# Kernel optimization log

Measured on AMD Instinct MI355X. Metric: run time of the kernel, lower is better.

Reference implementation:

```python
import jax, jax.numpy as jnp
import numpy as np

B, N, F_IN, F_OUT = 8, 2048, 64, 64
ALPHA = 0.2  # LeakyReLU negative slope


def setup_inputs() -> dict:
    key = jax.random.key(0)
    k_in, k_adj, k_w, k_a1, k_a2 = jax.random.split(key, 5)
    inp = jax.random.normal(k_in, (B, N, F_IN), dtype=jnp.float32)
    adj = (jax.random.uniform(k_adj, (B, N, N)) < 0.05).astype(jnp.float32)
    # xavier_uniform with gain=sqrt(2)
    def xavier(k, shape):
        fan_in, fan_out = shape[0], shape[1]
        bound = np.sqrt(2.0) * np.sqrt(6.0 / (fan_in + fan_out))
        return jax.random.uniform(k, shape, jnp.float32, -bound, bound)
    W = xavier(k_w, (F_IN, F_OUT))
    a1 = xavier(k_a1, (F_OUT, 1))
    a2 = xavier(k_a2, (F_OUT, 1))
    bias = jnp.full((N, F_OUT), 0.1, dtype=jnp.float32)
    return {"input": inp, "adj": adj, "W": W, "a1": a1, "a2": a2, "bias": bias}


def reference(input, adj, W, a1, a2, bias):
    # h: [B, N, F_OUT]
    h = jnp.einsum("bnf,fo->bno", input, W)
    f1 = h @ a1          # [B, N, 1]
    f2 = h @ a2          # [B, N, 1]
    e = jax.nn.leaky_relu(f1 + jnp.swapaxes(f2, 1, 2), negative_slope=ALPHA)  # [B, N, N]
    # NOTE: original multiplies adj elementwise (not -inf mask) and softmaxes over dim=1
    attention = jax.nn.softmax(adj * e, axis=1)
    h_prime = jnp.einsum("bij,bjo->bio", attention, h) + bias  # bias broadcasts over batch
    h_prime = h_prime + input  # in_features == out_features, no downsample
    return jax.nn.elu(h_prime)
```

## Files before the change

### kernel.cpp

```cpp
#include <hip/hip_runtime.h>
#include <cstdint>
#include <cstddef>

#define Bn 8
#define Nn 2048
#define Fn 64
#define ALPHA 0.2f

typedef __attribute__((ext_vector_type(8))) short  s8frag;
typedef __attribute__((ext_vector_type(4))) float  f4frag;

__device__ __forceinline__ float lrelu(float x) { return fmaxf(x, ALPHA * x); }
__device__ __forceinline__ float elu(float x)   { return x > 0.f ? x : __expf(x) - 1.f; }
__device__ __forceinline__ unsigned short bfr(float f) {
    unsigned u = __float_as_uint(f);
    u += 0x7fffu + ((u >> 16) & 1u);
    return (unsigned short)(u >> 16);
}

__global__ __launch_bounds__(256) void k1_h_f(
        const float* __restrict__ inp, const float* __restrict__ W,
        const float* __restrict__ a1, const float* __restrict__ a2,
        float* __restrict__ h, float* __restrict__ f1, float* __restrict__ f2) {
    __shared__ float Wl[Fn * Fn];
    __shared__ float inr[4 * Fn];
    int t = threadIdx.x;
    for (int k = t; k < Fn * Fn; k += 256) Wl[k] = W[k];
    size_t row0 = (size_t)blockIdx.x * 4;
    inr[t] = inp[row0 * Fn + t];
    __syncthreads();
    int r = t >> 6, o = t & 63;
    const float* irow = &inr[r * Fn];
    float acc = 0.f;
#pragma unroll
    for (int f = 0; f < Fn; ++f) acc = fmaf(irow[f], Wl[f * Fn + o], acc);
    size_t row = row0 + r;
    h[row * Fn + o] = acc;
    float p = acc * a1[o];
    float q = acc * a2[o];
#pragma unroll
    for (int off = 32; off > 0; off >>= 1) {
        p += __shfl_down(p, off, 64);
        q += __shfl_down(q, off, 64);
    }
    if (o == 0) { f1[row] = p; f2[row] = q; }
}

__global__ __launch_bounds__(256) void k1b_max(
        const float* __restrict__ f1, float* __restrict__ f1max) {
    int b = blockIdx.x, t = threadIdx.x;
    float m = -3.4e38f;
    for (int i = t; i < Nn; i += 256) m = fmaxf(m, f1[b * Nn + i]);
#pragma unroll
    for (int off = 32; off > 0; off >>= 1) m = fmaxf(m, __shfl_down(m, off, 64));
    __shared__ float sm[4];
    if ((t & 63) == 0) sm[t >> 6] = m;
    __syncthreads();
    if (t == 0) f1max[b] = fmaxf(fmaxf(sm[0], sm[1]), fmaxf(sm[2], sm[3]));
}

__global__ __launch_bounds__(512) void k2a_dense(
        const float* __restrict__ adj, const float* __restrict__ f1,
        const float* __restrict__ f2, const float* __restrict__ f1max_p,
        float* __restrict__ Dsum, unsigned short* __restrict__ P) {
    int b = blockIdx.x;
    int j0 = blockIdx.y * 256;
    int i0 = blockIdx.z * 128;
    int w = threadIdx.x >> 6, lane = threadIdx.x & 63;
    float f1max = f1max_p[b];
    float4 f2v = *(const float4*)&f2[b * Nn + j0 + 4 * lane];
    float Mf0 = fmaxf(lrelu(f1max + f2v.x), 0.f);
    float Mf1 = fmaxf(lrelu(f1max + f2v.y), 0.f);
    float Mf2 = fmaxf(lrelu(f1max + f2v.z), 0.f);
    float Mf3 = fmaxf(lrelu(f1max + f2v.w), 0.f);
    float s0 = 0.f, s1 = 0.f, s2 = 0.f, s3 = 0.f;
    const float* abase = adj + ((size_t)b * Nn) * Nn + j0 + 4 * lane;
    unsigned short* pbase = P + ((size_t)b * Nn) * Nn + j0 + 4 * lane;
    const float* f1b = f1 + b * Nn;

    for (int g = 0; g < 4; ++g) {
        int r0 = i0 + w + 32 * g;
        float4 av0 = *(const float4*)(abase + (size_t)(r0 +  0) * Nn);
        float4 av1 = *(const float4*)(abase + (size_t)(r0 +  8) * Nn);
        float4 av2 = *(const float4*)(abase + (size_t)(r0 + 16) * Nn);
        float4 av3 = *(const float4*)(abase + (size_t)(r0 + 24) * Nn);
        float fi0 = f1b[r0], fi1 = f1b[r0 + 8], fi2 = f1b[r0 + 16], fi3 = f1b[r0 + 24];
#define PROC(AV, FI, IROW)                                                     \
        {                                                                      \
            float e0 = __expf((AV.x != 0.f ? lrelu((FI) + f2v.x) : 0.f) - Mf0);\
            float e1 = __expf((AV.y != 0.f ? lrelu((FI) + f2v.y) : 0.f) - Mf1);\
            float e2 = __expf((AV.z != 0.f ? lrelu((FI) + f2v.z) : 0.f) - Mf2);\
            float e3 = __expf((AV.w != 0.f ? lrelu((FI) + f2v.w) : 0.f) - Mf3);\
            s0 += e0; s1 += e1; s2 += e2; s3 += e3;                            \
            uint2 pk;                                                          \
            pk.x = (unsigned)bfr(e0) | ((unsigned)bfr(e1) << 16);              \
            pk.y = (unsigned)bfr(e2) | ((unsigned)bfr(e3) << 16);              \
            *(uint2*)(pbase + (size_t)(IROW) * Nn) = pk;                       \
        }
        PROC(av0, fi0, r0 +  0)
        PROC(av1, fi1, r0 +  8)
        PROC(av2, fi2, r0 + 16)
        PROC(av3, fi3, r0 + 24)
#undef PROC
    }
    __shared__ float sred[8][256];
    sred[w][4 * lane + 0] = s0;
    sred[w][4 * lane + 1] = s1;
    sred[w][4 * lane + 2] = s2;
    sred[w][4 * lane + 3] = s3;
    __syncthreads();
    if (threadIdx.x < 256) {
        int c = threadIdx.x;
        float v = 0.f;
#pragma unroll
        for (int k = 0; k < 8; ++k) v += sred[k][c];
        atomicAdd(&Dsum[b * Nn + j0 + c], v);
    }
}

__global__ __launch_bounds__(256) void k2b_scale_T(
        const float* __restrict__ h, const float* __restrict__ Dsum,
        unsigned short* __restrict__ hTs) {
    int b = blockIdx.x;
    int j0 = blockIdx.y * 64;
    int t = threadIdx.x;
    __shared__ float Lh[64][68];
    __shared__ float Rsh[64];
    if (t < 64) Rsh[t] = 1.f / Dsum[b * Nn + j0 + t];
#pragma unroll
    for (int q = 0; q < 4; ++q) {
        int fi = t + 256 * q;
        int jj = fi >> 4, oq = fi & 15;
        float4 v = *(const float4*)(h + ((size_t)(b * Nn + j0 + jj)) * Fn + oq * 4);
        *(float4*)&Lh[jj][oq * 4] = v;
    }
    __syncthreads();
    int o = t >> 2, jg = (t & 3) * 16;
    unsigned wbuf[8];
#pragma unroll
    for (int s2 = 0; s2 < 8; ++s2) {
        int j = jg + 2 * s2;
        unsigned lo16 = bfr(Lh[j][o] * Rsh[j]);
        unsigned hi16 = bfr(Lh[j + 1][o] * Rsh[j + 1]);
        wbuf[s2] = lo16 | (hi16 << 16);
    }
    unsigned short* dst = hTs + ((size_t)(b * Fn + o)) * Nn + j0 + jg;
    *(uint4*)dst       = make_uint4(wbuf[0], wbuf[1], wbuf[2], wbuf[3]);
    *(uint4*)(dst + 8) = make_uint4(wbuf[4], wbuf[5], wbuf[6], wbuf[7]);
}

__global__ __launch_bounds__(256) void k3_gemm(
        const unsigned short* __restrict__ P, const unsigned short* __restrict__ hTs,
        const float* __restrict__ inp, const float* __restrict__ bias,
        float* __restrict__ out) {
    int b = blockIdx.x;
    int w = threadIdx.x >> 6, lane = threadIdx.x & 63;
    int laneM = lane & 15, laneK = (lane >> 4) * 8;
    int i0 = blockIdx.y * 32 + (w >> 1) * 16;
    int o0 = (w & 1) * 32;
    const unsigned short* A0 = hTs + ((size_t)(b * Fn + o0 + laneM)) * Nn + laneK;
    const unsigned short* A1 = A0 + 16 * Nn;
    const unsigned short* Bp = P + ((size_t)(b * Nn + i0 + laneM)) * Nn + laneK;

    f4frag c0 = {0.f, 0.f, 0.f, 0.f}, c1 = {0.f, 0.f, 0.f, 0.f};
    s8frag a0 = *(const s8frag*)A0;
    s8frag a1 = *(const s8frag*)A1;
    s8frag bb = *(const s8frag*)Bp;
#pragma unroll 4
    for (int k0 = 32; k0 < Nn; k0 += 32) {
        s8frag na0 = *(const s8frag*)(A0 + k0);
        s8frag na1 = *(const s8frag*)(A1 + k0);
        s8frag nbb = *(const s8frag*)(Bp + k0);
        c0 = __builtin_amdgcn_mfma_f32_16x16x32_bf16(a0, bb, c0, 0, 0, 0);
        c1 = __builtin_amdgcn_mfma_f32_16x16x32_bf16(a1, bb, c1, 0, 0, 0);
        a0 = na0; a1 = na1; bb = nbb;
    }
    c0 = __builtin_amdgcn_mfma_f32_16x16x32_bf16(a0, bb, c0, 0, 0, 0);
    c1 = __builtin_amdgcn_mfma_f32_16x16x32_bf16(a1, bb, c1, 0, 0, 0);

    int i = i0 + laneM;
    int oA = o0 + (lane >> 4) * 4;
    size_t gbase = ((size_t)b * Nn + i) * Fn;
    float4 in0 = *(const float4*)(inp + gbase + oA);
    float4 in1 = *(const float4*)(inp + gbase + oA + 16);
    float4 bi0 = *(const float4*)(bias + (size_t)i * Fn + oA);
    float4 bi1 = *(const float4*)(bias + (size_t)i * Fn + oA + 16);
    float4 r0v, r1v;
    r0v.x = elu(c0[0] + in0.x + bi0.x);
    r0v.y = elu(c0[1] + in0.y + bi0.y);
    r0v.z = elu(c0[2] + in0.z + bi0.z);
    r0v.w = elu(c0[3] + in0.w + bi0.w);
    r1v.x = elu(c1[0] + in1.x + bi1.x);
    r1v.y = elu(c1[1] + in1.y + bi1.y);
    r1v.z = elu(c1[2] + in1.z + bi1.z);
    r1v.w = elu(c1[3] + in1.w + bi1.w);
    *(float4*)(out + gbase + oA) = r0v;
    *(float4*)(out + gbase + oA + 16) = r1v;
}

extern "C" void kernel_launch(void* const* d_in, const int* in_sizes, int n_in,
                              void* d_out, int out_size, void* d_ws, size_t ws_size,
                              hipStream_t stream) {
    const float* inp  = (const float*)d_in[0];
    const float* adj  = (const float*)d_in[1];
    const float* W    = (const float*)d_in[2];
    const float* a1   = (const float*)d_in[3];
    const float* a2   = (const float*)d_in[4];
    const float* bias = (const float*)d_in[5];
    float* out = (float*)d_out;

    unsigned short* P   = (unsigned short*)d_ws;
    unsigned short* hTs = P + (size_t)Bn * Nn * Nn;
    float* h     = (float*)(hTs + (size_t)Bn * Fn * Nn);
    float* f1    = h + (size_t)Bn * Nn * Fn;
    float* f2    = f1 + (size_t)Bn * Nn;
    float* Dsum  = f2 + (size_t)Bn * Nn;
    float* f1max = Dsum + (size_t)Bn * Nn;

    hipMemsetAsync(Dsum, 0, (size_t)Bn * Nn * sizeof(float), stream);
    k1_h_f<<<Bn * Nn / 4, 256, 0, stream>>>(inp, W, a1, a2, h, f1, f2);
    k1b_max<<<Bn, 256, 0, stream>>>(f1, f1max);
    k2a_dense<<<dim3(Bn, Nn / 256, Nn / 128), 512, 0, stream>>>(adj, f1, f2, f1max, Dsum, P);
    k2b_scale_T<<<dim3(Bn, Nn / 64), 256, 0, stream>>>(h, Dsum, hTs);
    k3_gemm<<<dim3(Bn, Nn / 32), 256, 0, stream>>>(P, hTs, inp, bias, out);
}
```

Before: 277.1 us.

## Replace dense bf16 attention matrix with adjacency bitmask, recompute exps in GEMM

The first pass no longer writes the full bf16 exp matrix P. It stores a 1-bit-per-entry adjacency mask and still accumulates the column sums. The GEMM kernel rebuilds each exp on the fly from the mask, f1, and a per-column (f2, max) table staged in shared memory, then feeds the values straight into MFMA. This cuts the large P write and read by about 16x, at the cost of recomputing exp for every element in the GEMM, which now may be limited by ALU throughput.

```diff
diff --git a/kernel.cpp b/kernel.cpp
--- a/kernel.cpp
+++ b/kernel.cpp
@@ -59,12 +59,13 @@
     if (t == 0) f1max[b] = fmaxf(fmaxf(sm[0], sm[1]), fmaxf(sm[2], sm[3]));
 }
 
-__global__ __launch_bounds__(512) void k2a_dense(
+__global__ __launch_bounds__(512) void k2a_bits(
         const float* __restrict__ adj, const float* __restrict__ f1,
         const float* __restrict__ f2, const float* __restrict__ f1max_p,
-        float* __restrict__ Dsum, unsigned short* __restrict__ P) {
+        float* __restrict__ Dsum, unsigned char* __restrict__ bitsL) {
     int b = blockIdx.x;
-    int j0 = blockIdx.y * 256;
+    int cj = blockIdx.y;
+    int j0 = cj * 256;
     int i0 = blockIdx.z * 128;
     int w = threadIdx.x >> 6, lane = threadIdx.x & 63;
     float f1max = f1max_p[b];
@@ -75,11 +76,14 @@
     float Mf3 = fmaxf(lrelu(f1max + f2v.w), 0.f);
     float s0 = 0.f, s1 = 0.f, s2 = 0.f, s3 = 0.f;
     const float* abase = adj + ((size_t)b * Nn) * Nn + j0 + 4 * lane;
-    unsigned short* pbase = P + ((size_t)b * Nn) * Nn + j0 + 4 * lane;
     const float* f1b = f1 + b * Nn;
-
-    for (int g = 0; g < 4; ++g) {
-        int r0 = i0 + w + 32 * g;
+    int g = lane >> 1;
+    int boff = (g & 3) * 8 + (g >> 2);
+    bool evenlane = (lane & 1) == 0;
+    size_t bbase = ((size_t)(b * 8 + cj) * Nn) * 32;
+
+    for (int gi = 0; gi < 4; ++gi) {
+        int r0 = i0 + w + 32 * gi;
         float4 av0 = *(const float4*)(abase + (size_t)(r0 +  0) * Nn);
         float4 av1 = *(const float4*)(abase + (size_t)(r0 +  8) * Nn);
         float4 av2 = *(const float4*)(abase + (size_t)(r0 + 16) * Nn);
@@ -87,15 +91,18 @@
         float fi0 = f1b[r0], fi1 = f1b[r0 + 8], fi2 = f1b[r0 + 16], fi3 = f1b[r0 + 24];
 #define PROC(AV, FI, IROW)                                                     \
         {                                                                      \
-            float e0 = __expf((AV.x != 0.f ? lrelu((FI) + f2v.x) : 0.f) - Mf0);\
-            float e1 = __expf((AV.y != 0.f ? lrelu((FI) + f2v.y) : 0.f) - Mf1);\
-            float e2 = __expf((AV.z != 0.f ? lrelu((FI) + f2v.z) : 0.f) - Mf2);\
-            float e3 = __expf((AV.w != 0.f ? lrelu((FI) + f2v.w) : 0.f) - Mf3);\
-            s0 += e0; s1 += e1; s2 += e2; s3 += e3;                            \
-            uint2 pk;                                                          \
-            pk.x = (unsigned)bfr(e0) | ((unsigned)bfr(e1) << 16);              \
-            pk.y = (unsigned)bfr(e2) | ((unsigned)bfr(e3) << 16);              \
-            *(uint2*)(pbase + (size_t)(IROW) * Nn) = pk;                       \
+            bool n0 = AV.x != 0.f, n1 = AV.y != 0.f,                           \
+                 n2 = AV.z != 0.f, n3 = AV.w != 0.f;                           \
+            s0 += __expf((n0 ? lrelu((FI) + f2v.x) : 0.f) - Mf0);              \
+            s1 += __expf((n1 ? lrelu((FI) + f2v.y) : 0.f) - Mf1);              \
+            s2 += __expf((n2 ? lrelu((FI) + f2v.z) : 0.f) - Mf2);              \
+            s3 += __expf((n3 ? lrelu((FI) + f2v.w) : 0.f) - Mf3);              \
+            unsigned nib = (unsigned)n0 | ((unsigned)n1 << 1) |                \
+                           ((unsigned)n2 << 2) | ((unsigned)n3 << 3);          \
+            unsigned other = __shfl_xor(nib, 1, 64);                           \
+            if (evenlane)                                                      \
+                bitsL[bbase + (size_t)(IROW) * 32 + boff] =                    \
+                    (unsigned char)(nib | (other << 4));                       \
         }
         PROC(av0, fi0, r0 +  0)
         PROC(av1, fi1, r0 +  8)
@@ -120,13 +127,20 @@
 
 __global__ __launch_bounds__(256) void k2b_scale_T(
         const float* __restrict__ h, const float* __restrict__ Dsum,
-        unsigned short* __restrict__ hTs) {
+        const float* __restrict__ f2, const float* __restrict__ f1max_p,
+        unsigned short* __restrict__ hTs, float2* __restrict__ cf) {
     int b = blockIdx.x;
     int j0 = blockIdx.y * 64;
     int t = threadIdx.x;
     __shared__ float Lh[64][68];
     __shared__ float Rsh[64];
-    if (t < 64) Rsh[t] = 1.f / Dsum[b * Nn + j0 + t];
+    if (t < 64) {
+        int j = j0 + t;
+        float f2j = f2[b * Nn + j];
+        float Mf = fmaxf(lrelu(f1max_p[b] + f2j), 0.f);
+        Rsh[t] = 1.f / Dsum[b * Nn + j];
+        cf[b * Nn + j] = make_float2(f2j, Mf);
+    }
 #pragma unroll
     for (int q = 0; q < 4; ++q) {
         int fi = t + 256 * q;
@@ -149,53 +163,76 @@
     *(uint4*)(dst + 8) = make_uint4(wbuf[4], wbuf[5], wbuf[6], wbuf[7]);
 }
 
-__global__ __launch_bounds__(256) void k3_gemm(
-        const unsigned short* __restrict__ P, const unsigned short* __restrict__ hTs,
+__global__ __launch_bounds__(256) void k3_fused(
+        const unsigned char* __restrict__ bitsL,
+        const unsigned short* __restrict__ hTs,
+        const float2* __restrict__ cf, const float* __restrict__ f1,
         const float* __restrict__ inp, const float* __restrict__ bias,
         float* __restrict__ out) {
     int b = blockIdx.x;
+    int i0 = blockIdx.y * 64;
     int w = threadIdx.x >> 6, lane = threadIdx.x & 63;
-    int laneM = lane & 15, laneK = (lane >> 4) * 8;
-    int i0 = blockIdx.y * 32 + (w >> 1) * 16;
-    int o0 = (w & 1) * 32;
-    const unsigned short* A0 = hTs + ((size_t)(b * Fn + o0 + laneM)) * Nn + laneK;
-    const unsigned short* A1 = A0 + 16 * Nn;
-    const unsigned short* Bp = P + ((size_t)(b * Nn + i0 + laneM)) * Nn + laneK;
-
-    f4frag c0 = {0.f, 0.f, 0.f, 0.f}, c1 = {0.f, 0.f, 0.f, 0.f};
-    s8frag a0 = *(const s8frag*)A0;
-    s8frag a1 = *(const s8frag*)A1;
-    s8frag bb = *(const s8frag*)Bp;
-#pragma unroll 4
-    for (int k0 = 32; k0 < Nn; k0 += 32) {
-        s8frag na0 = *(const s8frag*)(A0 + k0);
-        s8frag na1 = *(const s8frag*)(A1 + k0);
-        s8frag nbb = *(const s8frag*)(Bp + k0);
-        c0 = __builtin_amdgcn_mfma_f32_16x16x32_bf16(a0, bb, c0, 0, 0, 0);
-        c1 = __builtin_amdgcn_mfma_f32_16x16x32_bf16(a1, bb, c1, 0, 0, 0);
-        a0 = na0; a1 = na1; bb = nbb;
-    }
-    c0 = __builtin_amdgcn_mfma_f32_16x16x32_bf16(a0, bb, c0, 0, 0, 0);
-    c1 = __builtin_amdgcn_mfma_f32_16x16x32_bf16(a1, bb, c1, 0, 0, 0);
-
-    int i = i0 + laneM;
-    int oA = o0 + (lane >> 4) * 4;
+    int m = lane & 15, kg = lane >> 4;
+    int i = i0 + w * 16 + m;
+
+    __shared__ float2 cfL[Nn];
+    {
+        const float4* src = (const float4*)(cf + (size_t)b * Nn);
+        float4* dst = (float4*)cfL;
+        for (int q = threadIdx.x; q < Nn / 2; q += 256) dst[q] = src[q];
+    }
+    uint2 pre[8];
+#pragma unroll
+    for (int jc = 0; jc < 8; ++jc)
+        pre[jc] = *(const uint2*)(bitsL + ((size_t)(b * 8 + jc) * Nn + i) * 32 + kg * 8);
+    float f1i = f1[b * Nn + i];
+    __syncthreads();
+
+    f4frag acc0 = {0.f,0.f,0.f,0.f}, acc1 = {0.f,0.f,0.f,0.f};
+    f4frag acc2 = {0.f,0.f,0.f,0.f}, acc3 = {0.f,0.f,0.f,0.f};
+    const unsigned short* Ab = hTs + (size_t)b * Fn * Nn + (size_t)m * Nn;
+
+    for (int jc = 0; jc < 8; ++jc) {
+        unsigned blo = pre[jc].x, bhi = pre[jc].y;
+#pragma unroll 2
+        for (int t = 0; t < 8; ++t) {
+            unsigned bv = ((t < 4 ? blo : bhi) >> ((t & 3) * 8)) & 0xffu;
+            int j = jc * 256 + t * 32 + kg * 8;
+            const float2* cp = &cfL[j];
+            s8frag bf;
+#pragma unroll
+            for (int r = 0; r < 8; ++r) {
+                float2 c = cp[r];
+                float l = lrelu(f1i + c.x);
+                float arg = (((bv >> r) & 1u) ? l : 0.f) - c.y;
+                bf[r] = (short)bfr(__expf(arg));
+            }
+            const unsigned short* Aj = Ab + j;
+            s8frag a0 = *(const s8frag*)(Aj);
+            s8frag a1 = *(const s8frag*)(Aj + 16 * Nn);
+            s8frag a2 = *(const s8frag*)(Aj + 32 * Nn);
+            s8frag a3 = *(const s8frag*)(Aj + 48 * Nn);
+            acc0 = __builtin_amdgcn_mfma_f32_16x16x32_bf16(a0, bf, acc0, 0, 0, 0);
+            acc1 = __builtin_amdgcn_mfma_f32_16x16x32_bf16(a1, bf, acc1, 0, 0, 0);
+            acc2 = __builtin_amdgcn_mfma_f32_16x16x32_bf16(a2, bf, acc2, 0, 0, 0);
+            acc3 = __builtin_amdgcn_mfma_f32_16x16x32_bf16(a3, bf, acc3, 0, 0, 0);
+        }
+    }
     size_t gbase = ((size_t)b * Nn + i) * Fn;
-    float4 in0 = *(const float4*)(inp + gbase + oA);
-    float4 in1 = *(const float4*)(inp + gbase + oA + 16);
-    float4 bi0 = *(const float4*)(bias + (size_t)i * Fn + oA);
-    float4 bi1 = *(const float4*)(bias + (size_t)i * Fn + oA + 16);
-    float4 r0v, r1v;
-    r0v.x = elu(c0[0] + in0.x + bi0.x);
-    r0v.y = elu(c0[1] + in0.y + bi0.y);
-    r0v.z = elu(c0[2] + in0.z + bi0.z);
-    r0v.w = elu(c0[3] + in0.w + bi0.w);
-    r1v.x = elu(c1[0] + in1.x + bi1.x);
-    r1v.y = elu(c1[1] + in1.y + bi1.y);
-    r1v.z = elu(c1[2] + in1.z + bi1.z);
-    r1v.w = elu(c1[3] + in1.w + bi1.w);
-    *(float4*)(out + gbase + oA) = r0v;
-    *(float4*)(out + gbase + oA + 16) = r1v;
+    int ob = kg * 4;
+    f4frag accs[4] = {acc0, acc1, acc2, acc3};
+#pragma unroll
+    for (int ot = 0; ot < 4; ++ot) {
+        int o = ot * 16 + ob;
+        float4 iv  = *(const float4*)(inp + gbase + o);
+        float4 bv4 = *(const float4*)(bias + (size_t)i * Fn + o);
+        float4 r;
+        r.x = elu(accs[ot][0] + iv.x + bv4.x);
+        r.y = elu(accs[ot][1] + iv.y + bv4.y);
+        r.z = elu(accs[ot][2] + iv.z + bv4.z);
+        r.w = elu(accs[ot][3] + iv.w + bv4.w);
+        *(float4*)(out + gbase + o) = r;
+    }
 }
 
 extern "C" void kernel_launch(void* const* d_in, const int* in_sizes, int n_in,
@@ -209,18 +246,19 @@
     const float* bias = (const float*)d_in[5];
     float* out = (float*)d_out;
 
-    unsigned short* P   = (unsigned short*)d_ws;
-    unsigned short* hTs = P + (size_t)Bn * Nn * Nn;
+    unsigned char* bitsL = (unsigned char*)d_ws;
+    unsigned short* hTs  = (unsigned short*)(bitsL + (size_t)Bn * Nn * Nn / 8);
     float* h     = (float*)(hTs + (size_t)Bn * Fn * Nn);
     float* f1    = h + (size_t)Bn * Nn * Fn;
     float* f2    = f1 + (size_t)Bn * Nn;
     float* Dsum  = f2 + (size_t)Bn * Nn;
-    float* f1max = Dsum + (size_t)Bn * Nn;
+    float2* cf   = (float2*)(Dsum + (size_t)Bn * Nn);
+    float* f1max = (float*)(cf + (size_t)Bn * Nn);
 
     hipMemsetAsync(Dsum, 0, (size_t)Bn * Nn * sizeof(float), stream);
     k1_h_f<<<Bn * Nn / 4, 256, 0, stream>>>(inp, W, a1, a2, h, f1, f2);
     k1b_max<<<Bn, 256, 0, stream>>>(f1, f1max);
-    k2a_dense<<<dim3(Bn, Nn / 256, Nn / 128), 512, 0, stream>>>(adj, f1, f2, f1max, Dsum, P);
-    k2b_scale_T<<<dim3(Bn, Nn / 64), 256, 0, stream>>>(h, Dsum, hTs);
-    k3_gemm<<<dim3(Bn, Nn / 32), 256, 0, stream>>>(P, hTs, inp, bias, out);
-}
+    k2a_bits<<<dim3(Bn, 8, 16), 512, 0, stream>>>(adj, f1, f2, f1max, Dsum, bitsL);
+    k2b_scale_T<<<dim3(Bn, Nn / 64), 256, 0, stream>>>(h, Dsum, f2, f1max, hTs, cf);
+    k3_fused<<<dim3(Bn, Nn / 64), 256, 0, stream>>>(bitsL, hTs, cf, f1, inp, bias, out);
+}
```

Result: faster. 260.9 us (-5.9%).
